# Kernel optimization log

Hardware: AMD Instinct MI355X
Metric: run time of the kernel (lower is better)

Reference implementation:

```python
import jax, jax.numpy as jnp
import numpy as np

N = 100000   # active voxels
K = 27       # 3x3x3 kernel offsets
C = 64       # in_channels == out_channels (residual block)
EPS = 1e-5


def setup_inputs() -> dict:
    key = jax.random.key(0)
    ks = jax.random.split(key, 10)
    feats = jax.random.normal(ks[0], (N, C), dtype=jnp.float32)
    # kernel-map: for each voxel, index of the neighbor voxel for each of the 27 offsets
    nbr = jax.random.randint(ks[1], (N, K), 0, N)
    nbr = nbr.at[:, K // 2].set(jnp.arange(N))  # center offset is identity
    w_scale = 1.0 / np.sqrt(K * C)
    W1 = jax.random.normal(ks[2], (K, C, C), dtype=jnp.float32) * w_scale
    b1 = jax.random.normal(ks[3], (C,), dtype=jnp.float32) * 0.01
    g1 = jnp.ones((C,), jnp.float32)
    be1 = jnp.zeros((C,), jnp.float32)
    W2 = jax.random.normal(ks[4], (K, C, C), dtype=jnp.float32) * w_scale
    b2 = jax.random.normal(ks[5], (C,), dtype=jnp.float32) * 0.01
    g2 = jnp.ones((C,), jnp.float32)
    be2 = jnp.zeros((C,), jnp.float32)
    return {"feats": feats, "nbr": nbr, "W1": W1, "b1": b1, "g1": g1, "be1": be1,
            "W2": W2, "b2": b2, "g2": g2, "be2": be2}


def _sparse_conv(f, nbr, W, b):
    # gather neighbor features per kernel offset: [N, K, C]
    g = f[nbr]
    # per-offset matmul and reduce over offsets (gather-matmul-scatter form)
    return jnp.einsum('nkc,kcd->nd', g, W) + b


def _bn(x, gamma, beta):
    # BatchNorm over active voxels (training-mode batch stats, per channel)
    mu = x.mean(axis=0)
    var = x.var(axis=0)
    return (x - mu) * jax.lax.rsqrt(var + EPS) * gamma + beta


def reference(feats, nbr, W1, b1, g1, be1, W2, b2, g2, be2):
    h = jax.nn.relu(_bn(_sparse_conv(feats, nbr, W1, b1), g1, be1))
    h = _bn(_sparse_conv(h, nbr, W2, b2), g2, be2)
    return jax.nn.relu(h + feats)  # residual add + ReLU
```

## Files before the change

kernel.cpp:

```cpp
#include <hip/hip_runtime.h>

#define NCH 64
#define KOFF 27
#define EPSV 1e-5f

typedef __attribute__((ext_vector_type(8))) short  bf16x8;
typedef __attribute__((ext_vector_type(4))) float  f32x4;
typedef __attribute__((ext_vector_type(8))) unsigned short u16x8;

__device__ __forceinline__ unsigned short f2bf(float x) {
    unsigned int u = __float_as_uint(x);
    u += 0x7fffu + ((u >> 16) & 1u);
    return (unsigned short)(u >> 16);
}

__global__ __launch_bounds__(256)
void prep_kernel(const float* __restrict__ feats,
                 const float* __restrict__ W1, const float* __restrict__ W2,
                 unsigned short* __restrict__ fbf,
                 unsigned short* __restrict__ wt1, unsigned short* __restrict__ wt2,
                 float* __restrict__ stat, int total8)
{
    const int b = blockIdx.x;
    if (b == 0) {
        stat[threadIdx.x] = 0.f;
        return;
    }
    if (b <= 108) {
        const float* W = (b <= 54) ? W1 : W2;
        unsigned short* Wt = (b <= 54) ? wt1 : wt2;
        const int t = (b <= 54 ? b - 1 : b - 55) * 256 + threadIdx.x;
        const int l  = t & 63;
        const int ct = (t >> 6) & 3;
        const int s  = (t >> 8) & 1;
        const int k  = t >> 9;
        const int d     = ct * 16 + (l & 15);
        const int cbase = s * 32 + (l >> 4) * 8;
        u16x8 o;
#pragma unroll
        for (int j = 0; j < 8; ++j)
            o[j] = f2bf(W[(size_t)k * 4096 + (size_t)(cbase + j) * 64 + d]);
        reinterpret_cast<u16x8*>(Wt)[t] = o;
        return;
    }
    const int idx = (b - 109) * 256 + threadIdx.x;
    if (idx >= total8) return;
    const float4* xp = reinterpret_cast<const float4*>(feats) + (size_t)idx * 2;
    const float4 a = xp[0], c = xp[1];
    u16x8 o;
    o[0] = f2bf(a.x); o[1] = f2bf(a.y); o[2] = f2bf(a.z); o[3] = f2bf(a.w);
    o[4] = f2bf(c.x); o[5] = f2bf(c.y); o[6] = f2bf(c.z); o[7] = f2bf(c.w);
    reinterpret_cast<u16x8*>(fbf)[idx] = o;
}

__global__ __launch_bounds__(64, 2)
void conv_mfma_kernel(const unsigned short* __restrict__ fin,
                      const int* __restrict__ nbr,
                      const unsigned short* __restrict__ Wt,
                      const float* __restrict__ bias,
                      float* __restrict__ out, float* __restrict__ stat, int N)
{
    __shared__ int s_idx[KOFF * 64 + 64];

    const int lane = threadIdx.x;
    const int n0   = blockIdx.x * 64;
    const int m    = lane & 15;
    const int quad = lane >> 4;

    {
        const int rem  = N - n0;
        const int maxi = (rem < 64 ? rem : 64) * KOFF;
        const int* nb  = nbr + (size_t)n0 * KOFF;
#pragma unroll
        for (int j = 0; j < KOFF; ++j) {
            const int p = j * 64 + lane;
            s_idx[p] = (p < maxi) ? nb[p] : 0;
        }
    }

    f32x4 acc[4][4];
#pragma unroll
    for (int mt = 0; mt < 4; ++mt)
#pragma unroll
        for (int ct = 0; ct < 4; ++ct) acc[mt][ct] = (f32x4){0.f, 0.f, 0.f, 0.f};

    bf16x8 A[2][4][2];
    bf16x8 B[2][2][4];

#define LOADK(k, p)                                                          \
    {                                                                        \
        _Pragma("unroll")                                                    \
        for (int mt = 0; mt < 4; ++mt) {                                     \
            const int r = s_idx[(mt * 16 + m) * KOFF + (k)];                 \
            const unsigned short* fp = fin + (size_t)r * NCH + quad * 8;     \
            A[p][mt][0] = *reinterpret_cast<const bf16x8*>(fp);              \
            A[p][mt][1] = *reinterpret_cast<const bf16x8*>(fp + 32);         \
        }                                                                    \
        const unsigned short* wp = Wt + (size_t)(k) * 4096 + lane * 8;       \
        _Pragma("unroll")                                                    \
        for (int s = 0; s < 2; ++s)                                          \
            _Pragma("unroll")                                                \
            for (int ct = 0; ct < 4; ++ct)                                   \
                B[p][s][ct] =                                                \
                    *reinterpret_cast<const bf16x8*>(wp + (s * 4 + ct) * 512);\
    }

#define DOMFMA(p)                                                            \
    {                                                                        \
        _Pragma("unroll")                                                    \
        for (int mt = 0; mt < 4; ++mt)                                       \
            _Pragma("unroll")                                                \
            for (int s = 0; s < 2; ++s)                                      \
                _Pragma("unroll")                                            \
                for (int ct = 0; ct < 4; ++ct)                               \
                    acc[mt][ct] = __builtin_amdgcn_mfma_f32_16x16x32_bf16(   \
                        A[p][mt][s], B[p][s][ct], acc[mt][ct], 0, 0, 0);     \
    }

    LOADK(0, 0);
#pragma unroll 1
    for (int k = 0; k < KOFF - 1; k += 2) {
        LOADK(k + 1, 1);
        DOMFMA(0);
        LOADK(k + 2, 0);
        DOMFMA(1);
    }
    DOMFMA(0);

#pragma unroll
    for (int ct = 0; ct < 4; ++ct) {
        const int ch = ct * 16 + m;
        const float bv = bias[ch];
        float s = 0.f, q = 0.f;
#pragma unroll
        for (int mt = 0; mt < 4; ++mt) {
#pragma unroll
            for (int r = 0; r < 4; ++r) {
                const int vox = n0 + mt * 16 + quad * 4 + r;
                if (vox < N) {
                    const float v = acc[mt][ct][r] + bv;
                    out[(size_t)vox * NCH + ch] = v;
                    s += v;
                    q += v * v;
                }
            }
        }
        s += __shfl_xor(s, 16, 64);
        s += __shfl_xor(s, 32, 64);
        q += __shfl_xor(q, 16, 64);
        q += __shfl_xor(q, 32, 64);
        if (quad == 0) {
            atomicAdd(&stat[ch], s);
            atomicAdd(&stat[64 + ch], q);
        }
    }
#undef LOADK
#undef DOMFMA
}

__global__ __launch_bounds__(256)
void bn_relu_bf16_kernel(const float* __restrict__ x, const float* __restrict__ sums,
                         const float* __restrict__ gmm, const float* __restrict__ bet,
                         float invN, unsigned short* __restrict__ y, int total8)
{
    const int idx = blockIdx.x * 256 + threadIdx.x;
    if (idx >= total8) return;
    const int c0 = (idx & 7) * 8;
    const float4* xp = reinterpret_cast<const float4*>(x) + (size_t)idx * 2;
    const float4 a = xp[0], b = xp[1];
    float v[8] = {a.x, a.y, a.z, a.w, b.x, b.y, b.z, b.w};
    u16x8 o;
#pragma unroll
    for (int i = 0; i < 8; ++i) {
        const int c = c0 + i;
        const float mu  = sums[c] * invN;
        const float var = sums[64 + c] * invN - mu * mu;
        const float rs  = rsqrtf(var + EPSV);
        const float sc  = gmm[c] * rs;
        const float sh  = bet[c] - mu * sc;
        o[i] = f2bf(fmaxf(fmaf(v[i], sc, sh), 0.f));
    }
    reinterpret_cast<u16x8*>(y)[idx] = o;
}

__global__ __launch_bounds__(256)
void bn_res_relu_kernel(float* __restrict__ x, const float* __restrict__ feats,
                        const float* __restrict__ sums, const float* __restrict__ gmm,
                        const float* __restrict__ bet, float invN, int total4)
{
    const int idx = blockIdx.x * blockDim.x + threadIdx.x;
    if (idx >= total4) return;
    float4 v = reinterpret_cast<float4*>(x)[idx];
    const float4 f = reinterpret_cast<const float4*>(feats)[idx];
    const int c0 = (idx & 15) * 4;
    float sc[4], sh[4];
#pragma unroll
    for (int i = 0; i < 4; ++i) {
        const int c = c0 + i;
        const float mu  = sums[c] * invN;
        const float var = sums[64 + c] * invN - mu * mu;
        const float rs  = rsqrtf(var + EPSV);
        sc[i] = gmm[c] * rs;
        sh[i] = bet[c] - mu * sc[i];
    }
    v.x = fmaxf(fmaf(v.x, sc[0], sh[0]) + f.x, 0.f);
    v.y = fmaxf(fmaf(v.y, sc[1], sh[1]) + f.y, 0.f);
    v.z = fmaxf(fmaf(v.z, sc[2], sh[2]) + f.z, 0.f);
    v.w = fmaxf(fmaf(v.w, sc[3], sh[3]) + f.w, 0.f);
    reinterpret_cast<float4*>(x)[idx] = v;
}

extern "C" void kernel_launch(void* const* d_in, const int* in_sizes, int n_in,
                              void* d_out, int out_size, void* d_ws, size_t ws_size,
                              hipStream_t stream)
{
    const float* feats = (const float*)d_in[0];
    const int*   nbr   = (const int*)d_in[1];
    const float* W1    = (const float*)d_in[2];
    const float* b1    = (const float*)d_in[3];
    const float* g1    = (const float*)d_in[4];
    const float* be1   = (const float*)d_in[5];
    const float* W2    = (const float*)d_in[6];
    const float* b2    = (const float*)d_in[7];
    const float* g2    = (const float*)d_in[8];
    const float* be2   = (const float*)d_in[9];
    float* out = (float*)d_out;

    const int N  = in_sizes[0] / NCH;
    const int NC = N * NCH;
    const float invN = 1.0f / (float)N;

    float*          h0   = (float*)d_ws;
    unsigned short* fbf  = (unsigned short*)(h0 + NC);
    unsigned short* hbf  = fbf + NC;
    unsigned short* wt1  = hbf + NC;
    unsigned short* wt2  = wt1 + KOFF * 4096;
    float*          stat = (float*)(wt2 + KOFF * 4096);

    const int total8   = NC / 8;
    const int castGrid = (total8 + 255) / 256;
    const int prepGrid = 1 + 108 + castGrid;
    const int convGrid = (N + 63) / 64;

    prep_kernel<<<prepGrid, 256, 0, stream>>>(feats, W1, W2, fbf, wt1, wt2,
                                              stat, total8);
    conv_mfma_kernel<<<convGrid, 64, 0, stream>>>(fbf, nbr, wt1, b1, h0, stat, N);
    bn_relu_bf16_kernel<<<castGrid, 256, 0, stream>>>(h0, stat, g1, be1, invN,
                                                      hbf, total8);
    conv_mfma_kernel<<<convGrid, 64, 0, stream>>>(hbf, nbr, wt2, b2, out,
                                                  stat + 128, N);
    bn_res_relu_kernel<<<(NC / 4 + 255) / 256, 256, 0, stream>>>(
        out, feats, stat + 128, g2, be2, invN, NC / 4);
}
```

Baseline: 322.8 us.

## Split conv kernel offsets across four wavefronts with LDS reduction

The sparse conv kernel now launches 256 threads per 64-voxel tile. Each of the four wavefronts handles an interleaved subset of the 27 kernel offsets, and the partial accumulators are combined through a two-step shared-memory tree before wave 0 writes outputs and BN stats. Neighbor indices are pre-scaled to byte offsets in LDS, removing a multiply from the gather path. This shortens the serial MFMA/gather chain per tile and adds latency hiding. The cost is about 42KB of LDS per block, which limits occupancy, plus two barriers and idle waves during the epilogue.

```diff
diff --git a/kernel.cpp b/kernel.cpp
--- a/kernel.cpp
+++ b/kernel.cpp
@@ -53,16 +53,19 @@
     reinterpret_cast<u16x8*>(fbf)[idx] = o;
 }
 
-__global__ __launch_bounds__(64, 2)
+__global__ __launch_bounds__(256, 2)
 void conv_mfma_kernel(const unsigned short* __restrict__ fin,
                       const int* __restrict__ nbr,
                       const unsigned short* __restrict__ Wt,
                       const float* __restrict__ bias,
                       float* __restrict__ out, float* __restrict__ stat, int N)
 {
-    __shared__ int s_idx[KOFF * 64 + 64];
-
-    const int lane = threadIdx.x;
+    __shared__ int   s_idx[KOFF * 64];
+    __shared__ float red[2][64 * 68];
+
+    const int t    = threadIdx.x;
+    const int lane = t & 63;
+    const int w    = t >> 6;
     const int n0   = blockIdx.x * 64;
     const int m    = lane & 15;
     const int quad = lane >> 4;
@@ -71,12 +74,10 @@
         const int rem  = N - n0;
         const int maxi = (rem < 64 ? rem : 64) * KOFF;
         const int* nb  = nbr + (size_t)n0 * KOFF;
-#pragma unroll
-        for (int j = 0; j < KOFF; ++j) {
-            const int p = j * 64 + lane;
-            s_idx[p] = (p < maxi) ? nb[p] : 0;
-        }
-    }
+        for (int p = t; p < KOFF * 64; p += 256)
+            s_idx[p] = ((p < maxi) ? nb[p] : 0) * (NCH * 2);
+    }
+    __syncthreads();
 
     f32x4 acc[4][4];
 #pragma unroll
@@ -86,17 +87,18 @@
 
     bf16x8 A[2][4][2];
     bf16x8 B[2][2][4];
-
-#define LOADK(k, p)                                                          \
+    const char* finB = (const char*)fin;
+
+#define LOADK(kk, p)                                                         \
     {                                                                        \
         _Pragma("unroll")                                                    \
         for (int mt = 0; mt < 4; ++mt) {                                     \
-            const int r = s_idx[(mt * 16 + m) * KOFF + (k)];                 \
-            const unsigned short* fp = fin + (size_t)r * NCH + quad * 8;     \
+            const int ofs = s_idx[(mt * 16 + m) * KOFF + (kk)];              \
+            const char* fp = finB + ofs + quad * 16;                         \
             A[p][mt][0] = *reinterpret_cast<const bf16x8*>(fp);              \
-            A[p][mt][1] = *reinterpret_cast<const bf16x8*>(fp + 32);         \
+            A[p][mt][1] = *reinterpret_cast<const bf16x8*>(fp + 64);         \
         }                                                                    \
-        const unsigned short* wp = Wt + (size_t)(k) * 4096 + lane * 8;       \
+        const unsigned short* wp = Wt + (size_t)(kk) * 4096 + lane * 8;      \
         _Pragma("unroll")                                                    \
         for (int s = 0; s < 2; ++s)                                          \
             _Pragma("unroll")                                                \
@@ -117,45 +119,87 @@
                         A[p][mt][s], B[p][s][ct], acc[mt][ct], 0, 0, 0);     \
     }
 
-    LOADK(0, 0);
+    const int kstart = 3 - w;
+    const int nk     = (w == 0) ? 6 : 7;
+
+    LOADK(kstart, 0);
+    int j = 0;
 #pragma unroll 1
-    for (int k = 0; k < KOFF - 1; k += 2) {
-        LOADK(k + 1, 1);
+    for (; j + 2 < nk; j += 2) {
+        LOADK(kstart + 4 * (j + 1), 1);
         DOMFMA(0);
-        LOADK(k + 2, 0);
+        LOADK(kstart + 4 * (j + 2), 0);
         DOMFMA(1);
     }
-    DOMFMA(0);
-
-#pragma unroll
-    for (int ct = 0; ct < 4; ++ct) {
-        const int ch = ct * 16 + m;
-        const float bv = bias[ch];
-        float s = 0.f, q = 0.f;
-#pragma unroll
-        for (int mt = 0; mt < 4; ++mt) {
-#pragma unroll
-            for (int r = 0; r < 4; ++r) {
-                const int vox = n0 + mt * 16 + quad * 4 + r;
-                if (vox < N) {
-                    const float v = acc[mt][ct][r] + bv;
-                    out[(size_t)vox * NCH + ch] = v;
-                    s += v;
-                    q += v * v;
+    if (nk - j == 2) {
+        LOADK(kstart + 4 * (j + 1), 1);
+        DOMFMA(0);
+        DOMFMA(1);
+    } else {
+        DOMFMA(0);
+    }
+
+#define WRITE_ACC(buf)                                                       \
+    {                                                                        \
+        _Pragma("unroll")                                                    \
+        for (int mt = 0; mt < 4; ++mt)                                       \
+            _Pragma("unroll")                                                \
+            for (int ct = 0; ct < 4; ++ct)                                   \
+                *reinterpret_cast<f32x4*>(                                   \
+                    &buf[(ct * 16 + m) * 68 + mt * 16 + quad * 4]) =         \
+                    acc[mt][ct];                                             \
+    }
+#define READ_ADD(buf)                                                        \
+    {                                                                        \
+        _Pragma("unroll")                                                    \
+        for (int mt = 0; mt < 4; ++mt)                                       \
+            _Pragma("unroll")                                                \
+            for (int ct = 0; ct < 4; ++ct)                                   \
+                acc[mt][ct] += *reinterpret_cast<const f32x4*>(              \
+                    &buf[(ct * 16 + m) * 68 + mt * 16 + quad * 4]);          \
+    }
+
+    if (w == 1) WRITE_ACC(red[0])
+    else if (w == 3) WRITE_ACC(red[1])
+    __syncthreads();
+    if (w == 0) READ_ADD(red[0])
+    else if (w == 2) { READ_ADD(red[1]) WRITE_ACC(red[1]) }
+    __syncthreads();
+
+    if (w == 0) {
+        READ_ADD(red[1])
+#pragma unroll
+        for (int ct = 0; ct < 4; ++ct) {
+            const int ch = ct * 16 + m;
+            const float bv = bias[ch];
+            float s = 0.f, q = 0.f;
+#pragma unroll
+            for (int mt = 0; mt < 4; ++mt) {
+#pragma unroll
+                for (int r = 0; r < 4; ++r) {
+                    const int vox = n0 + mt * 16 + quad * 4 + r;
+                    if (vox < N) {
+                        const float v = acc[mt][ct][r] + bv;
+                        out[(size_t)vox * NCH + ch] = v;
+                        s += v;
+                        q += v * v;
+                    }
                 }
             }
-        }
-        s += __shfl_xor(s, 16, 64);
-        s += __shfl_xor(s, 32, 64);
-        q += __shfl_xor(q, 16, 64);
-        q += __shfl_xor(q, 32, 64);
-        if (quad == 0) {
-            atomicAdd(&stat[ch], s);
-            atomicAdd(&stat[64 + ch], q);
+            s += __shfl_xor(s, 16, 64);
+            s += __shfl_xor(s, 32, 64);
+            q += __shfl_xor(q, 16, 64);
+            q += __shfl_xor(q, 32, 64);
+            if (quad == 0) {
+                atomicAdd(&stat[ch], s);
+                atomicAdd(&stat[64 + ch], q);
+            }
         }
     }
 #undef LOADK
 #undef DOMFMA
+#undef WRITE_ACC
+#undef READ_ADD
 }
 
 __global__ __launch_bounds__(256)
@@ -244,11 +288,11 @@
 
     prep_kernel<<<prepGrid, 256, 0, stream>>>(feats, W1, W2, fbf, wt1, wt2,
                                               stat, total8);
-    conv_mfma_kernel<<<convGrid, 64, 0, stream>>>(fbf, nbr, wt1, b1, h0, stat, N);
+    conv_mfma_kernel<<<convGrid, 256, 0, stream>>>(fbf, nbr, wt1, b1, h0, stat, N);
     bn_relu_bf16_kernel<<<castGrid, 256, 0, stream>>>(h0, stat, g1, be1, invN,
                                                       hbf, total8);
-    conv_mfma_kernel<<<convGrid, 64, 0, stream>>>(hbf, nbr, wt2, b2, out,
-                                                  stat + 128, N);
+    conv_mfma_kernel<<<convGrid, 256, 0, stream>>>(hbf, nbr, wt2, b2, out,
+                                                   stat + 128, N);
     bn_res_relu_kernel<<<(NC / 4 + 255) / 256, 256, 0, stream>>>(
         out, feats, stat + 128, g2, be2, invN, NC / 4);
 }
```

Result: no change. 321.3 us (-0.5%).

## Halve conv voxel tile and replace stat atomics with partial-sum reduction

Applied to the files above, without the earlier changes.

Each conv block now processes 32 voxels instead of 64. This doubles the grid, shrinks the accumulator and A-register footprint, and raises the launch-bounds occupancy hint from 2 to 3, so more waves are in flight to hide gather latency. Per-block BN sums are written to a scratch buffer and summed by a new small reduction kernel, replacing global atomics. Neighbor indices are prescaled into byte offsets in shared memory. In exchange, each voxel gets less reuse of the weight loads, and two extra kernel launches are added.

```diff
diff --git a/kernel.cpp b/kernel.cpp
--- a/kernel.cpp
+++ b/kernel.cpp
@@ -53,50 +53,48 @@
     reinterpret_cast<u16x8*>(fbf)[idx] = o;
 }
 
-__global__ __launch_bounds__(64, 2)
+__global__ __launch_bounds__(64, 3)
 void conv_mfma_kernel(const unsigned short* __restrict__ fin,
                       const int* __restrict__ nbr,
                       const unsigned short* __restrict__ Wt,
                       const float* __restrict__ bias,
-                      float* __restrict__ out, float* __restrict__ stat, int N)
-{
-    __shared__ int s_idx[KOFF * 64 + 64];
+                      float* __restrict__ out, float* __restrict__ pstat, int N)
+{
+    __shared__ int s_idx[32 * KOFF];
 
     const int lane = threadIdx.x;
-    const int n0   = blockIdx.x * 64;
+    const int n0   = blockIdx.x * 32;
     const int m    = lane & 15;
     const int quad = lane >> 4;
 
     {
         const int rem  = N - n0;
-        const int maxi = (rem < 64 ? rem : 64) * KOFF;
+        const int maxi = (rem < 32 ? rem : 32) * KOFF;
         const int* nb  = nbr + (size_t)n0 * KOFF;
-#pragma unroll
-        for (int j = 0; j < KOFF; ++j) {
-            const int p = j * 64 + lane;
-            s_idx[p] = (p < maxi) ? nb[p] : 0;
-        }
-    }
-
-    f32x4 acc[4][4];
-#pragma unroll
-    for (int mt = 0; mt < 4; ++mt)
+        for (int p = lane; p < 32 * KOFF; p += 64)
+            s_idx[p] = ((p < maxi) ? nb[p] : 0) * (NCH * 2);
+    }
+
+    f32x4 acc[2][4];
+#pragma unroll
+    for (int mt = 0; mt < 2; ++mt)
 #pragma unroll
         for (int ct = 0; ct < 4; ++ct) acc[mt][ct] = (f32x4){0.f, 0.f, 0.f, 0.f};
 
-    bf16x8 A[2][4][2];
+    bf16x8 A[2][2][2];
     bf16x8 B[2][2][4];
-
-#define LOADK(k, p)                                                          \
+    const char* finB = (const char*)fin;
+
+#define LOADK(kk, p)                                                         \
     {                                                                        \
         _Pragma("unroll")                                                    \
-        for (int mt = 0; mt < 4; ++mt) {                                     \
-            const int r = s_idx[(mt * 16 + m) * KOFF + (k)];                 \
-            const unsigned short* fp = fin + (size_t)r * NCH + quad * 8;     \
+        for (int mt = 0; mt < 2; ++mt) {                                     \
+            const int ofs = s_idx[(mt * 16 + m) * KOFF + (kk)];              \
+            const char* fp = finB + ofs + quad * 16;                         \
             A[p][mt][0] = *reinterpret_cast<const bf16x8*>(fp);              \
-            A[p][mt][1] = *reinterpret_cast<const bf16x8*>(fp + 32);         \
+            A[p][mt][1] = *reinterpret_cast<const bf16x8*>(fp + 64);         \
         }                                                                    \
-        const unsigned short* wp = Wt + (size_t)(k) * 4096 + lane * 8;       \
+        const unsigned short* wp = Wt + (size_t)(kk) * 4096 + lane * 8;      \
         _Pragma("unroll")                                                    \
         for (int s = 0; s < 2; ++s)                                          \
             _Pragma("unroll")                                                \
@@ -108,7 +106,7 @@
 #define DOMFMA(p)                                                            \
     {                                                                        \
         _Pragma("unroll")                                                    \
-        for (int mt = 0; mt < 4; ++mt)                                       \
+        for (int mt = 0; mt < 2; ++mt)                                       \
             _Pragma("unroll")                                                \
             for (int s = 0; s < 2; ++s)                                      \
                 _Pragma("unroll")                                            \
@@ -119,7 +117,7 @@
 
     LOADK(0, 0);
 #pragma unroll 1
-    for (int k = 0; k < KOFF - 1; k += 2) {
+    for (int k = 0; k + 2 < KOFF; k += 2) {
         LOADK(k + 1, 1);
         DOMFMA(0);
         LOADK(k + 2, 0);
@@ -133,7 +131,7 @@
         const float bv = bias[ch];
         float s = 0.f, q = 0.f;
 #pragma unroll
-        for (int mt = 0; mt < 4; ++mt) {
+        for (int mt = 0; mt < 2; ++mt) {
 #pragma unroll
             for (int r = 0; r < 4; ++r) {
                 const int vox = n0 + mt * 16 + quad * 4 + r;
@@ -150,12 +148,29 @@
         q += __shfl_xor(q, 16, 64);
         q += __shfl_xor(q, 32, 64);
         if (quad == 0) {
-            atomicAdd(&stat[ch], s);
-            atomicAdd(&stat[64 + ch], q);
+            float* pr = pstat + (size_t)blockIdx.x * 128;
+            pr[ch]      = s;
+            pr[64 + ch] = q;
         }
     }
 #undef LOADK
 #undef DOMFMA
+}
+
+__global__ __launch_bounds__(256)
+void reduce_stats_kernel(const float* __restrict__ pstat, float* __restrict__ stat,
+                         int rows)
+{
+    __shared__ float s_[256];
+    const int ch = threadIdx.x & 127;
+    const int h  = threadIdx.x >> 7;
+    float acc = 0.f;
+    for (int r = blockIdx.x * 2 + h; r < rows; r += gridDim.x * 2)
+        acc += pstat[(size_t)r * 128 + ch];
+    s_[threadIdx.x] = acc;
+    __syncthreads();
+    if (threadIdx.x < 128)
+        atomicAdd(&stat[threadIdx.x], s_[threadIdx.x] + s_[threadIdx.x + 128]);
 }
 
 __global__ __launch_bounds__(256)
@@ -240,15 +255,21 @@
     const int total8   = NC / 8;
     const int castGrid = (total8 + 255) / 256;
     const int prepGrid = 1 + 108 + castGrid;
-    const int convGrid = (N + 63) / 64;
+    const int convGrid = (N + 31) / 32;
+
+    float* pstat1 = out;
+    float* pstat2 = h0;
 
     prep_kernel<<<prepGrid, 256, 0, stream>>>(feats, W1, W2, fbf, wt1, wt2,
                                               stat, total8);
-    conv_mfma_kernel<<<convGrid, 64, 0, stream>>>(fbf, nbr, wt1, b1, h0, stat, N);
+    conv_mfma_kernel<<<convGrid, 64, 0, stream>>>(fbf, nbr, wt1, b1, h0,
+                                                  pstat1, N);
+    reduce_stats_kernel<<<32, 256, 0, stream>>>(pstat1, stat, convGrid);
     bn_relu_bf16_kernel<<<castGrid, 256, 0, stream>>>(h0, stat, g1, be1, invN,
                                                       hbf, total8);
     conv_mfma_kernel<<<convGrid, 64, 0, stream>>>(hbf, nbr, wt2, b2, out,
-                                                  stat + 128, N);
+                                                  pstat2, N);
+    reduce_stats_kernel<<<32, 256, 0, stream>>>(pstat2, stat + 128, convGrid);
     bn_res_relu_kernel<<<(NC / 4 + 255) / 256, 256, 0, stream>>>(
         out, feats, stat + 128, g2, be2, invN, NC / 4);
 }
```

Result: faster. 296.6 us (-8.1%).

## Stage gathered rows and weights into LDS with a 4-deep async pipeline

Applied to the files above, without the earlier changes.

The conv kernel now uses global_load_lds to copy the gathered neighbor feature rows and per-offset weights asynchronously into a 4-slot LDS ring, with an XOR swizzle to avoid bank conflicts. The index table is transposed and pre-scaled to byte offsets. This replaces the 2-deep register double buffering, so more gather loads are in flight and memory latency is hidden behind the MFMAs. In exchange each block uses about 71 KB of LDS, which may cut occupancy, and correctness depends on the hand-tuned vmcnt waits.

```diff
diff --git a/kernel.cpp b/kernel.cpp
--- a/kernel.cpp
+++ b/kernel.cpp
@@ -3,6 +3,7 @@
 #define NCH 64
 #define KOFF 27
 #define EPSV 1e-5f
+#define DSLOT 4
 
 typedef __attribute__((ext_vector_type(8))) short  bf16x8;
 typedef __attribute__((ext_vector_type(4))) float  f32x4;
@@ -60,12 +61,16 @@
                       const float* __restrict__ bias,
                       float* __restrict__ out, float* __restrict__ stat, int N)
 {
-    __shared__ int s_idx[KOFF * 64 + 64];
+    __shared__ __align__(16) unsigned short sA[DSLOT * 4096];
+    __shared__ __align__(16) unsigned short sB[DSLOT * 4096];
+    __shared__ int s_idx[KOFF * 64];
 
     const int lane = threadIdx.x;
     const int n0   = blockIdx.x * 64;
     const int m    = lane & 15;
     const int quad = lane >> 4;
+    const int rsel = lane >> 3;
+    const int vchunk = (((lane & 7) ^ (rsel & 7)) << 4);
 
     {
         const int rem  = N - n0;
@@ -73,59 +78,93 @@
         const int* nb  = nbr + (size_t)n0 * KOFF;
 #pragma unroll
         for (int j = 0; j < KOFF; ++j) {
-            const int p = j * 64 + lane;
-            s_idx[p] = (p < maxi) ? nb[p] : 0;
+            const int p   = j * 64 + lane;
+            const int row = p / KOFF;
+            const int kk  = p - row * KOFF;
+            s_idx[kk * 64 + row] = ((p < maxi) ? nb[p] : 0) * (NCH * 2);
         }
     }
 
+    const char* fbfB = (const char*)fin;
+    const char* WtB  = (const char*)Wt;
+
+    int offA[4][2];
+#pragma unroll
+    for (int mt = 0; mt < 4; ++mt)
+#pragma unroll
+        for (int sf = 0; sf < 2; ++sf)
+            offA[mt][sf] = (mt * 16 + m) * 128 + (((quad + 4 * sf) ^ (m & 7)) << 4);
+    const int offBbase = lane * 16;
+
     f32x4 acc[4][4];
 #pragma unroll
     for (int mt = 0; mt < 4; ++mt)
 #pragma unroll
         for (int ct = 0; ct < 4; ++ct) acc[mt][ct] = (f32x4){0.f, 0.f, 0.f, 0.f};
 
-    bf16x8 A[2][4][2];
-    bf16x8 B[2][2][4];
-
-#define LOADK(k, p)                                                          \
-    {                                                                        \
-        _Pragma("unroll")                                                    \
-        for (int mt = 0; mt < 4; ++mt) {                                     \
-            const int r = s_idx[(mt * 16 + m) * KOFF + (k)];                 \
-            const unsigned short* fp = fin + (size_t)r * NCH + quad * 8;     \
-            A[p][mt][0] = *reinterpret_cast<const bf16x8*>(fp);              \
-            A[p][mt][1] = *reinterpret_cast<const bf16x8*>(fp + 32);         \
-        }                                                                    \
-        const unsigned short* wp = Wt + (size_t)(k) * 4096 + lane * 8;       \
-        _Pragma("unroll")                                                    \
-        for (int s = 0; s < 2; ++s)                                          \
-            _Pragma("unroll")                                                \
-            for (int ct = 0; ct < 4; ++ct)                                   \
-                B[p][s][ct] =                                                \
-                    *reinterpret_cast<const bf16x8*>(wp + (s * 4 + ct) * 512);\
-    }
-
-#define DOMFMA(p)                                                            \
-    {                                                                        \
-        _Pragma("unroll")                                                    \
-        for (int mt = 0; mt < 4; ++mt)                                       \
-            _Pragma("unroll")                                                \
-            for (int s = 0; s < 2; ++s)                                      \
-                _Pragma("unroll")                                            \
-                for (int ct = 0; ct < 4; ++ct)                               \
-                    acc[mt][ct] = __builtin_amdgcn_mfma_f32_16x16x32_bf16(   \
-                        A[p][mt][s], B[p][s][ct], acc[mt][ct], 0, 0, 0);     \
-    }
-
-    LOADK(0, 0);
-#pragma unroll 1
-    for (int k = 0; k < KOFF - 1; k += 2) {
-        LOADK(k + 1, 1);
-        DOMFMA(0);
-        LOADK(k + 2, 0);
-        DOMFMA(1);
-    }
-    DOMFMA(0);
+#define STAGE(kk)                                                             \
+    {                                                                         \
+        const int slot_ = (kk) & (DSLOT - 1);                                 \
+        _Pragma("unroll")                                                     \
+        for (int i_ = 0; i_ < 8; ++i_) {                                      \
+            const int ofs_ = s_idx[(kk) * 64 + i_ * 8 + rsel];                \
+            __builtin_amdgcn_global_load_lds(                                 \
+                (const __attribute__((address_space(1))) void*)               \
+                    (fbfB + (unsigned)(ofs_ + vchunk)),                       \
+                (__attribute__((address_space(3))) void*)                     \
+                    ((char*)sA + slot_ * 8192 + i_ * 1024),                   \
+                16, 0, 0);                                                    \
+        }                                                                     \
+        _Pragma("unroll")                                                     \
+        for (int i_ = 0; i_ < 8; ++i_) {                                      \
+            __builtin_amdgcn_global_load_lds(                                 \
+                (const __attribute__((address_space(1))) void*)               \
+                    (WtB + (kk) * 8192 + i_ * 1024 + offBbase),               \
+                (__attribute__((address_space(3))) void*)                     \
+                    ((char*)sB + slot_ * 8192 + i_ * 1024),                   \
+                16, 0, 0);                                                    \
+        }                                                                     \
+    }
+
+#define STEP(kk, vm)                                                          \
+    {                                                                         \
+        asm volatile("s_waitcnt vmcnt(%0)" :: "i"(vm) : "memory");            \
+        const int slot_ = (kk) & (DSLOT - 1);                                 \
+        bf16x8 Af[4][2], Bf[2][4];                                            \
+        _Pragma("unroll")                                                     \
+        for (int mt = 0; mt < 4; ++mt)                                        \
+            _Pragma("unroll")                                                 \
+            for (int sf = 0; sf < 2; ++sf)                                    \
+                Af[mt][sf] = *reinterpret_cast<const bf16x8*>(                \
+                    (const char*)sA + slot_ * 8192 + offA[mt][sf]);           \
+        _Pragma("unroll")                                                     \
+        for (int sf = 0; sf < 2; ++sf)                                        \
+            _Pragma("unroll")                                                 \
+            for (int ct = 0; ct < 4; ++ct)                                    \
+                Bf[sf][ct] = *reinterpret_cast<const bf16x8*>(                \
+                    (const char*)sB + slot_ * 8192 + (sf * 4 + ct) * 1024 +   \
+                    offBbase);                                                \
+        asm volatile("s_waitcnt lgkmcnt(0)" ::: "memory");                    \
+        if ((kk) + DSLOT < KOFF) STAGE((kk) + DSLOT)                          \
+        _Pragma("unroll")                                                     \
+        for (int mt = 0; mt < 4; ++mt)                                        \
+            _Pragma("unroll")                                                 \
+            for (int sf = 0; sf < 2; ++sf)                                    \
+                _Pragma("unroll")                                             \
+                for (int ct = 0; ct < 4; ++ct)                                \
+                    acc[mt][ct] = __builtin_amdgcn_mfma_f32_16x16x32_bf16(    \
+                        Af[mt][sf], Bf[sf][ct], acc[mt][ct], 0, 0, 0);        \
+    }
+
+    STAGE(0) STAGE(1) STAGE(2) STAGE(3)
+    STEP(0, 48)  STEP(1, 48)  STEP(2, 48)  STEP(3, 48)  STEP(4, 48)
+    STEP(5, 48)  STEP(6, 48)  STEP(7, 48)  STEP(8, 48)  STEP(9, 48)
+    STEP(10, 48) STEP(11, 48) STEP(12, 48) STEP(13, 48) STEP(14, 48)
+    STEP(15, 48) STEP(16, 48) STEP(17, 48) STEP(18, 48) STEP(19, 48)
+    STEP(20, 48) STEP(21, 48) STEP(22, 48) STEP(23, 48)
+    STEP(24, 32) STEP(25, 16) STEP(26, 0)
+#undef STAGE
+#undef STEP
 
 #pragma unroll
     for (int ct = 0; ct < 4; ++ct) {
@@ -154,8 +193,6 @@
             atomicAdd(&stat[64 + ch], q);
         }
     }
-#undef LOADK
-#undef DOMFMA
 }
 
 __global__ __launch_bounds__(256)
@@ -244,7 +281,8 @@
 
     prep_kernel<<<prepGrid, 256, 0, stream>>>(feats, W1, W2, fbf, wt1, wt2,
                                               stat, total8);
-    conv_mfma_kernel<<<convGrid, 64, 0, stream>>>(fbf, nbr, wt1, b1, h0, stat, N);
+    conv_mfma_kernel<<<convGrid, 64, 0, stream>>>(fbf, nbr, wt1, b1, h0,
+                                                  stat, N);
     bn_relu_bf16_kernel<<<castGrid, 256, 0, stream>>>(h0, stat, g1, be1, invN,
                                                       hbf, total8);
     conv_mfma_kernel<<<convGrid, 64, 0, stream>>>(hbf, nbr, wt2, b2, out,
```

Result: slower. 373.2 us (+15.6%).
